# Kernel optimization log

Measured on AMD Instinct MI355X. Metric: run time of the kernel, lower is better.

## Reference

```python
import jax, jax.numpy as jnp
import numpy as np

MARGIN = 0.1
N_SUBSETS = 3
NEG_INF = -1e30


def setup_inputs() -> dict:
    key = jax.random.key(0)
    k1, k2 = jax.random.split(key)
    B, D = 12288, 128
    emb = jax.random.normal(k1, (B, D), dtype=jnp.float32)
    emb = emb / jnp.linalg.norm(emb, axis=-1, keepdims=True)  # cosine-style sims in [-1,1]
    target = jax.random.randint(k2, (B,), 0, 512, dtype=jnp.int64)
    return {"emb": emb, "target": target}


def _subset_loss(e, t):
    # e: [m, D], t: [m]
    m = e.shape[0]
    sim = e @ e.T                                   # [m, m]
    same = t[:, None] == t[None, :]
    eye = jnp.eye(m, dtype=bool)
    pos = same & ~eye                                # positives, diagonal excluded
    neg = ~same                                      # negatives (diag is 'same', so excluded)
    max_neg = jnp.max(jnp.where(neg, sim, NEG_INF), axis=1)   # neg_pair_[-1]
    max_pos = jnp.max(jnp.where(pos, sim, NEG_INF), axis=1)   # pos_pair_[-1]
    # select pos sims < max_neg + margin; loss = sum(1 - pos)
    pos_sel = pos & (sim < (max_neg + MARGIN)[:, None])
    pos_loss = jnp.sum(jnp.where(pos_sel, 1.0 - sim, 0.0), axis=1)
    # select neg sims > max(0.6, max_pos) - margin; loss = sum(neg)
    thr = jnp.maximum(jnp.float32(0.6), max_pos) - MARGIN
    neg_sel = neg & (sim > thr[:, None])
    neg_loss = jnp.sum(jnp.where(neg_sel, sim, 0.0), axis=1)
    has_pos = jnp.any(pos, axis=1)
    row_loss = jnp.where(has_pos, pos_loss + neg_loss, 0.0)
    return jnp.mean(row_loss)  # sum(loss)/n


def reference(emb, target):
    B, D = emb.shape
    m = B // N_SUBSETS
    e = emb.reshape(N_SUBSETS, m, D)
    t = target.reshape(N_SUBSETS, m)
    losses = jax.vmap(_subset_loss)(e, t)  # [n_subsets]
    return jnp.mean(losses)
```

## Files before the change

### kernel.cpp

```cpp
#include <hip/hip_runtime.h>
#include <stdint.h>

typedef __bf16 bf16x8 __attribute__((ext_vector_type(8)));
typedef float f32x4 __attribute__((ext_vector_type(4)));
typedef unsigned short ushort8v __attribute__((ext_vector_type(8)));

static constexpr int SUBSETS = 3;
static constexpr int M = 4096;
static constexpr int D = 128;

static constexpr int WG_ROWS = 256;
static constexpr int WG_COLS = 256;
static constexpr int NSTRIP = M / WG_COLS;
static constexpr int NPANEL = M / WG_ROWS;
static constexpr int WGS = SUBSETS * NPANEL * NSTRIP;
static constexpr int SCOLS = 32;
static constexpr int NSTAGE = WG_COLS / SCOLS;

#define MARGIN_F 0.1f
#define NEGINF (-1e30f)
#define POSINF (1e30f)

__global__ void cvt_f32_bf16(const float* __restrict__ in,
                             unsigned short* __restrict__ out, int n8,
                             float* __restrict__ loss_out) {
    int i = blockIdx.x * blockDim.x + threadIdx.x;
    if (i == 0) *loss_out = 0.0f;
    if (i >= n8) return;
    const float4* p = reinterpret_cast<const float4*>(in) + (size_t)i * 2;
    float4 a = p[0];
    float4 b = p[1];
    float v[8] = {a.x, a.y, a.z, a.w, b.x, b.y, b.z, b.w};
    ushort8v r;
#pragma unroll
    for (int j = 0; j < 8; ++j) {
        uint32_t u = __builtin_bit_cast(uint32_t, v[j]);
        u = (u + 0x7FFFu + ((u >> 16) & 1u)) >> 16;
        r[j] = (unsigned short)u;
    }
    *(reinterpret_cast<ushort8v*>(out) + i) = r;
}

__device__ __forceinline__ void stage_tile(const unsigned short* __restrict__ base,
                                           unsigned short* __restrict__ ldsbuf,
                                           int w, int lane) {
#pragma unroll
    for (int i = 0; i < 2; ++i) {
        const int slocal = w * 2048 + i * 1024 + lane * 16;
        const int col = slocal >> 8;
        const int off = (slocal & 255) ^ ((col & 7) << 4);
        const char* gsrc = (const char*)base + col * 256 + off;
        char* ldst = (char*)ldsbuf + w * 2048 + i * 1024;
        __builtin_amdgcn_global_load_lds(
            (const __attribute__((address_space(1))) void*)gsrc,
            (__attribute__((address_space(3))) void*)ldst,
            16, 0, 0);
    }
}

__device__ __forceinline__ bf16x8 lds_bfrag(const unsigned short* __restrict__ ldsbuf,
                                            int tt, int llo, int lhi, int kb) {
    const int col = tt * 16 + llo;
    const int off = (kb * 64 + lhi * 16) ^ ((col & 7) << 4);
    return *reinterpret_cast<const bf16x8*>((const char*)ldsbuf + col * 256 + off);
}

__global__ __launch_bounds__(256) void pass_max(
        const unsigned short* __restrict__ ebf,
        const int* __restrict__ tgt,
        float* __restrict__ wsmax) {
    __shared__ unsigned short lds[2][SCOLS * D];

    const int wg = blockIdx.x;
    const int s = wg >> 8;
    const int rem = wg & 255;
    const int panel = rem & (NPANEL - 1);
    const int cs = rem >> 4;

    const int tid = threadIdx.x;
    const int w = tid >> 6, lane = tid & 63;
    const int lhi = lane >> 4, llo = lane & 15;

    const unsigned short* E = ebf + (size_t)s * M * D;
    const int* T = tgt + s * M;
    const int rowBase = panel * WG_ROWS + w * 64;
    const int colBase = cs * WG_COLS;

    stage_tile(E + (size_t)colBase * D, lds[0], w, lane);

    bf16x8 a[4][4];
#pragma unroll
    for (int rr = 0; rr < 4; ++rr) {
        const int row = rowBase + rr * 16 + llo;
#pragma unroll
        for (int kb = 0; kb < 4; ++kb)
            a[rr][kb] = *reinterpret_cast<const bf16x8*>(
                E + (size_t)row * D + kb * 32 + lhi * 8);
    }
    int trow[4][4];
#pragma unroll
    for (int rr = 0; rr < 4; ++rr)
#pragma unroll
        for (int r = 0; r < 4; ++r)
            trow[rr][r] = T[rowBase + rr * 16 + lhi * 4 + r];

    float mp[4][4], mn[4][4];
#pragma unroll
    for (int rr = 0; rr < 4; ++rr)
#pragma unroll
        for (int r = 0; r < 4; ++r) { mp[rr][r] = NEGINF; mn[rr][r] = NEGINF; }

    __syncthreads();

    for (int st = 0; st < NSTAGE; ++st) {
        const int buf = st & 1;
        if (st + 1 < NSTAGE)
            stage_tile(E + (size_t)(colBase + (st + 1) * SCOLS) * D, lds[buf ^ 1], w, lane);
#pragma unroll
        for (int tt = 0; tt < 2; ++tt) {
            const int bcol = colBase + st * SCOLS + tt * 16 + llo;
            bf16x8 b[4];
#pragma unroll
            for (int kb = 0; kb < 4; ++kb) b[kb] = lds_bfrag(lds[buf], tt, llo, lhi, kb);
            const int tcol = T[bcol];
#pragma unroll
            for (int rr = 0; rr < 4; ++rr) {
                f32x4 acc = {0.f, 0.f, 0.f, 0.f};
#pragma unroll
                for (int kb = 0; kb < 4; ++kb)
                    acc = __builtin_amdgcn_mfma_f32_16x16x32_bf16(a[rr][kb], b[kb], acc, 0, 0, 0);
#pragma unroll
                for (int r = 0; r < 4; ++r) {
                    const float sv = acc[r];
                    const int rowG = rowBase + rr * 16 + lhi * 4 + r;
                    const bool same = (tcol == trow[rr][r]);
                    const bool offd = (rowG != bcol);
                    mp[rr][r] = fmaxf(mp[rr][r], (same && offd) ? sv : NEGINF);
                    mn[rr][r] = fmaxf(mn[rr][r], same ? NEGINF : sv);
                }
            }
        }
        __syncthreads();
    }

#pragma unroll
    for (int rr = 0; rr < 4; ++rr)
#pragma unroll
        for (int r = 0; r < 4; ++r) {
#pragma unroll
            for (int off = 1; off < 16; off <<= 1) {
                mp[rr][r] = fmaxf(mp[rr][r], __shfl_xor(mp[rr][r], off));
                mn[rr][r] = fmaxf(mn[rr][r], __shfl_xor(mn[rr][r], off));
            }
        }
    if (llo == 0) {
#pragma unroll
        for (int rr = 0; rr < 4; ++rr)
#pragma unroll
            for (int r = 0; r < 4; ++r) {
                const int row = rowBase + rr * 16 + lhi * 4 + r;
                wsmax[((size_t)(0 * SUBSETS + s) * M + row) * NSTRIP + cs] = mp[rr][r];
                wsmax[((size_t)(1 * SUBSETS + s) * M + row) * NSTRIP + cs] = mn[rr][r];
            }
    }
}

__global__ __launch_bounds__(256) void pass_sum(
        const unsigned short* __restrict__ ebf,
        const int* __restrict__ tgt,
        const float* __restrict__ wsmax,
        float* __restrict__ out) {
    __shared__ unsigned short lds[2][SCOLS * D];
    __shared__ float wsum[4];

    const int wg = blockIdx.x;
    const int s = wg >> 8;
    const int rem = wg & 255;
    const int panel = rem & (NPANEL - 1);
    const int cs = rem >> 4;

    const int tid = threadIdx.x;
    const int w = tid >> 6, lane = tid & 63;
    const int lhi = lane >> 4, llo = lane & 15;

    const unsigned short* E = ebf + (size_t)s * M * D;
    const int* T = tgt + s * M;
    const int rowBase = panel * WG_ROWS + w * 64;
    const int colBase = cs * WG_COLS;

    stage_tile(E + (size_t)colBase * D, lds[0], w, lane);

    float thrP[4][4], thrN[4][4];
#pragma unroll
    for (int rr = 0; rr < 4; ++rr)
#pragma unroll
        for (int r = 0; r < 4; ++r) {
            const int row = rowBase + rr * 16 + lhi * 4 + r;
            float vp = wsmax[((size_t)(0 * SUBSETS + s) * M + row) * NSTRIP + llo];
            float vn = wsmax[((size_t)(1 * SUBSETS + s) * M + row) * NSTRIP + llo];
#pragma unroll
            for (int off = 1; off < 16; off <<= 1) {
                vp = fmaxf(vp, __shfl_xor(vp, off));
                vn = fmaxf(vn, __shfl_xor(vn, off));
            }
            const bool hasPos = (vp > -1e29f);
            thrP[rr][r] = hasPos ? vn + MARGIN_F : NEGINF;
            thrN[rr][r] = hasPos ? fmaxf(0.6f, vp) - MARGIN_F : POSINF;
        }

    bf16x8 a[4][4];
#pragma unroll
    for (int rr = 0; rr < 4; ++rr) {
        const int row = rowBase + rr * 16 + llo;
#pragma unroll
        for (int kb = 0; kb < 4; ++kb)
            a[rr][kb] = *reinterpret_cast<const bf16x8*>(
                E + (size_t)row * D + kb * 32 + lhi * 8);
    }
    int trow[4][4];
#pragma unroll
    for (int rr = 0; rr < 4; ++rr)
#pragma unroll
        for (int r = 0; r < 4; ++r)
            trow[rr][r] = T[rowBase + rr * 16 + lhi * 4 + r];

    float acl[4][4];
#pragma unroll
    for (int rr = 0; rr < 4; ++rr)
#pragma unroll
        for (int r = 0; r < 4; ++r) acl[rr][r] = 0.f;

    __syncthreads();

    for (int st = 0; st < NSTAGE; ++st) {
        const int buf = st & 1;
        if (st + 1 < NSTAGE)
            stage_tile(E + (size_t)(colBase + (st + 1) * SCOLS) * D, lds[buf ^ 1], w, lane);
#pragma unroll
        for (int tt = 0; tt < 2; ++tt) {
            const int bcol = colBase + st * SCOLS + tt * 16 + llo;
            bf16x8 b[4];
#pragma unroll
            for (int kb = 0; kb < 4; ++kb) b[kb] = lds_bfrag(lds[buf], tt, llo, lhi, kb);
            const int tcol = T[bcol];
#pragma unroll
            for (int rr = 0; rr < 4; ++rr) {
                f32x4 acc = {0.f, 0.f, 0.f, 0.f};
#pragma unroll
                for (int kb = 0; kb < 4; ++kb)
                    acc = __builtin_amdgcn_mfma_f32_16x16x32_bf16(a[rr][kb], b[kb], acc, 0, 0, 0);
#pragma unroll
                for (int r = 0; r < 4; ++r) {
                    const float sv = acc[r];
                    const int rowG = rowBase + rr * 16 + lhi * 4 + r;
                    const bool same = (tcol == trow[rr][r]);
                    const bool offd = (rowG != bcol);
                    const float addp = (same && offd && (sv < thrP[rr][r])) ? (1.0f - sv) : 0.0f;
                    const float addn = (!same && (sv > thrN[rr][r])) ? sv : 0.0f;
                    acl[rr][r] += addp + addn;
                }
            }
        }
        __syncthreads();
    }

    float tot = 0.f;
#pragma unroll
    for (int rr = 0; rr < 4; ++rr)
#pragma unroll
        for (int r = 0; r < 4; ++r) tot += acl[rr][r];
#pragma unroll
    for (int off = 1; off < 64; off <<= 1) tot += __shfl_xor(tot, off);

    if (lane == 0) wsum[w] = tot;
    __syncthreads();
    if (tid == 0)
        atomicAdd(out, (wsum[0] + wsum[1] + wsum[2] + wsum[3]) * (1.0f / 12288.0f));
}

extern "C" void kernel_launch(void* const* d_in, const int* in_sizes, int n_in,
                              void* d_out, int out_size, void* d_ws, size_t ws_size,
                              hipStream_t stream) {
    const float* emb = (const float*)d_in[0];
    const int* tgt = (const int*)d_in[1];
    float* out = (float*)d_out;

    unsigned short* ebf = (unsigned short*)d_ws;
    float* wsmax = (float*)((char*)d_ws + (size_t)SUBSETS * M * D * 2);

    const int n = SUBSETS * M * D;
    const int n8 = n / 8;

    cvt_f32_bf16<<<n8 / 256, 256, 0, stream>>>(emb, ebf, n8, out);
    pass_max<<<WGS, 256, 0, stream>>>(ebf, tgt, wsmax);
    pass_sum<<<WGS, 256, 0, stream>>>(ebf, tgt, wsmax, out);
}
```

Before: 126.2 us.

## Drop LDS staging; load B fragments directly from global with register double-buffering

Removes the shared-memory tile staging and workgroup barriers in both passes; each wave now independently loads its column fragments straight from global memory (relying on L1/L2 caching) with a two-deep register prefetch, and waves in a workgroup no longer share a column strip. Occupancy hint of 3 blocks per SIMD is added and the per-block LDS reduction is replaced with a per-wave atomicAdd. It aims to remove barrier stalls and LDS traffic, at the cost of redundant global/L2 reads of the B tiles, more atomics, and less data reuse across waves.

```diff
diff --git a/kernel.cpp b/kernel.cpp
--- a/kernel.cpp
+++ b/kernel.cpp
@@ -9,13 +9,13 @@
 static constexpr int M = 4096;
 static constexpr int D = 128;
 
-static constexpr int WG_ROWS = 256;
-static constexpr int WG_COLS = 256;
-static constexpr int NSTRIP = M / WG_COLS;
-static constexpr int NPANEL = M / WG_ROWS;
-static constexpr int WGS = SUBSETS * NPANEL * NSTRIP;
-static constexpr int SCOLS = 32;
-static constexpr int NSTAGE = WG_COLS / SCOLS;
+static constexpr int RPW = 64;
+static constexpr int CPW = 256;
+static constexpr int NSTRIP = M / CPW;
+static constexpr int NRJ = M / RPW;
+static constexpr int WAVES_TOTAL = SUBSETS * NRJ * NSTRIP;
+static constexpr int WGS = WAVES_TOTAL / 4;
+static constexpr int NST = CPW / 16;
 
 #define MARGIN_F 0.1f
 #define NEGINF (-1e30f)
@@ -41,52 +41,22 @@
     *(reinterpret_cast<ushort8v*>(out) + i) = r;
 }
 
-__device__ __forceinline__ void stage_tile(const unsigned short* __restrict__ base,
-                                           unsigned short* __restrict__ ldsbuf,
-                                           int w, int lane) {
-#pragma unroll
-    for (int i = 0; i < 2; ++i) {
-        const int slocal = w * 2048 + i * 1024 + lane * 16;
-        const int col = slocal >> 8;
-        const int off = (slocal & 255) ^ ((col & 7) << 4);
-        const char* gsrc = (const char*)base + col * 256 + off;
-        char* ldst = (char*)ldsbuf + w * 2048 + i * 1024;
-        __builtin_amdgcn_global_load_lds(
-            (const __attribute__((address_space(1))) void*)gsrc,
-            (__attribute__((address_space(3))) void*)ldst,
-            16, 0, 0);
-    }
-}
-
-__device__ __forceinline__ bf16x8 lds_bfrag(const unsigned short* __restrict__ ldsbuf,
-                                            int tt, int llo, int lhi, int kb) {
-    const int col = tt * 16 + llo;
-    const int off = (kb * 64 + lhi * 16) ^ ((col & 7) << 4);
-    return *reinterpret_cast<const bf16x8*>((const char*)ldsbuf + col * 256 + off);
-}
-
-__global__ __launch_bounds__(256) void pass_max(
+__global__ __launch_bounds__(256, 3) void pass_max(
         const unsigned short* __restrict__ ebf,
         const int* __restrict__ tgt,
         float* __restrict__ wsmax) {
-    __shared__ unsigned short lds[2][SCOLS * D];
-
-    const int wg = blockIdx.x;
-    const int s = wg >> 8;
-    const int rem = wg & 255;
-    const int panel = rem & (NPANEL - 1);
-    const int cs = rem >> 4;
-
-    const int tid = threadIdx.x;
-    const int w = tid >> 6, lane = tid & 63;
+    const int gwid = blockIdx.x * 4 + (threadIdx.x >> 6);
+    const int lane = threadIdx.x & 63;
+    const int s = gwid >> 10;
+    const int rem = gwid & 1023;
+    const int rj = rem & (NRJ - 1);
+    const int cs = rem >> 6;
     const int lhi = lane >> 4, llo = lane & 15;
 
     const unsigned short* E = ebf + (size_t)s * M * D;
     const int* T = tgt + s * M;
-    const int rowBase = panel * WG_ROWS + w * 64;
-    const int colBase = cs * WG_COLS;
-
-    stage_tile(E + (size_t)colBase * D, lds[0], w, lane);
+    const int rowBase = rj * RPW;
+    const int colBase = cs * CPW;
 
     bf16x8 a[4][4];
 #pragma unroll
@@ -110,37 +80,44 @@
 #pragma unroll
         for (int r = 0; r < 4; ++r) { mp[rr][r] = NEGINF; mn[rr][r] = NEGINF; }
 
-    __syncthreads();
-
-    for (int st = 0; st < NSTAGE; ++st) {
-        const int buf = st & 1;
-        if (st + 1 < NSTAGE)
-            stage_tile(E + (size_t)(colBase + (st + 1) * SCOLS) * D, lds[buf ^ 1], w, lane);
-#pragma unroll
-        for (int tt = 0; tt < 2; ++tt) {
-            const int bcol = colBase + st * SCOLS + tt * 16 + llo;
-            bf16x8 b[4];
-#pragma unroll
-            for (int kb = 0; kb < 4; ++kb) b[kb] = lds_bfrag(lds[buf], tt, llo, lhi, kb);
-            const int tcol = T[bcol];
-#pragma unroll
-            for (int rr = 0; rr < 4; ++rr) {
-                f32x4 acc = {0.f, 0.f, 0.f, 0.f};
-#pragma unroll
-                for (int kb = 0; kb < 4; ++kb)
-                    acc = __builtin_amdgcn_mfma_f32_16x16x32_bf16(a[rr][kb], b[kb], acc, 0, 0, 0);
-#pragma unroll
-                for (int r = 0; r < 4; ++r) {
-                    const float sv = acc[r];
-                    const int rowG = rowBase + rr * 16 + lhi * 4 + r;
-                    const bool same = (tcol == trow[rr][r]);
-                    const bool offd = (rowG != bcol);
-                    mp[rr][r] = fmaxf(mp[rr][r], (same && offd) ? sv : NEGINF);
-                    mn[rr][r] = fmaxf(mn[rr][r], same ? NEGINF : sv);
-                }
-            }
-        }
-        __syncthreads();
+    auto loadB = [&](bf16x8 (&dst)[4], int st) {
+        const unsigned short* bp = E + (size_t)(colBase + st * 16 + llo) * D + lhi * 8;
+#pragma unroll
+        for (int kb = 0; kb < 4; ++kb)
+            dst[kb] = *reinterpret_cast<const bf16x8*>(bp + kb * 32);
+    };
+    auto proc = [&](int st, bf16x8 (&b)[4], int tcol) {
+        const int bcol = colBase + st * 16 + llo;
+#pragma unroll
+        for (int rr = 0; rr < 4; ++rr) {
+            f32x4 acc = {0.f, 0.f, 0.f, 0.f};
+#pragma unroll
+            for (int kb = 0; kb < 4; ++kb)
+                acc = __builtin_amdgcn_mfma_f32_16x16x32_bf16(a[rr][kb], b[kb], acc, 0, 0, 0);
+#pragma unroll
+            for (int r = 0; r < 4; ++r) {
+                const float sv = acc[r];
+                const int rowG = rowBase + rr * 16 + lhi * 4 + r;
+                const bool same = (tcol == trow[rr][r]);
+                const bool offd = (rowG != bcol);
+                mp[rr][r] = fmaxf(mp[rr][r], (same && offd) ? sv : NEGINF);
+                mn[rr][r] = fmaxf(mn[rr][r], same ? NEGINF : sv);
+            }
+        }
+    };
+
+    bf16x8 bA[4], bB[4];
+    int tcA, tcB;
+    loadB(bA, 0);
+    tcA = T[colBase + llo];
+#pragma unroll
+    for (int st2 = 0; st2 < NST; st2 += 2) {
+        if (st2 + 1 < NST) { loadB(bB, st2 + 1); tcB = T[colBase + (st2 + 1) * 16 + llo]; }
+        proc(st2, bA, tcA);
+        if (st2 + 1 < NST) {
+            if (st2 + 2 < NST) { loadB(bA, st2 + 2); tcA = T[colBase + (st2 + 2) * 16 + llo]; }
+            proc(st2 + 1, bB, tcB);
+        }
     }
 
 #pragma unroll
@@ -165,30 +142,23 @@
     }
 }
 
-__global__ __launch_bounds__(256) void pass_sum(
+__global__ __launch_bounds__(256, 3) void pass_sum(
         const unsigned short* __restrict__ ebf,
         const int* __restrict__ tgt,
         const float* __restrict__ wsmax,
         float* __restrict__ out) {
-    __shared__ unsigned short lds[2][SCOLS * D];
-    __shared__ float wsum[4];
-
-    const int wg = blockIdx.x;
-    const int s = wg >> 8;
-    const int rem = wg & 255;
-    const int panel = rem & (NPANEL - 1);
-    const int cs = rem >> 4;
-
-    const int tid = threadIdx.x;
-    const int w = tid >> 6, lane = tid & 63;
+    const int gwid = blockIdx.x * 4 + (threadIdx.x >> 6);
+    const int lane = threadIdx.x & 63;
+    const int s = gwid >> 10;
+    const int rem = gwid & 1023;
+    const int rj = rem & (NRJ - 1);
+    const int cs = rem >> 6;
     const int lhi = lane >> 4, llo = lane & 15;
 
     const unsigned short* E = ebf + (size_t)s * M * D;
     const int* T = tgt + s * M;
-    const int rowBase = panel * WG_ROWS + w * 64;
-    const int colBase = cs * WG_COLS;
-
-    stage_tile(E + (size_t)colBase * D, lds[0], w, lane);
+    const int rowBase = rj * RPW;
+    const int colBase = cs * CPW;
 
     float thrP[4][4], thrN[4][4];
 #pragma unroll
@@ -224,58 +194,52 @@
         for (int r = 0; r < 4; ++r)
             trow[rr][r] = T[rowBase + rr * 16 + lhi * 4 + r];
 
-    float acl[4][4];
-#pragma unroll
-    for (int rr = 0; rr < 4; ++rr)
-#pragma unroll
-        for (int r = 0; r < 4; ++r) acl[rr][r] = 0.f;
-
-    __syncthreads();
-
-    for (int st = 0; st < NSTAGE; ++st) {
-        const int buf = st & 1;
-        if (st + 1 < NSTAGE)
-            stage_tile(E + (size_t)(colBase + (st + 1) * SCOLS) * D, lds[buf ^ 1], w, lane);
-#pragma unroll
-        for (int tt = 0; tt < 2; ++tt) {
-            const int bcol = colBase + st * SCOLS + tt * 16 + llo;
-            bf16x8 b[4];
-#pragma unroll
-            for (int kb = 0; kb < 4; ++kb) b[kb] = lds_bfrag(lds[buf], tt, llo, lhi, kb);
-            const int tcol = T[bcol];
-#pragma unroll
-            for (int rr = 0; rr < 4; ++rr) {
-                f32x4 acc = {0.f, 0.f, 0.f, 0.f};
-#pragma unroll
-                for (int kb = 0; kb < 4; ++kb)
-                    acc = __builtin_amdgcn_mfma_f32_16x16x32_bf16(a[rr][kb], b[kb], acc, 0, 0, 0);
-#pragma unroll
-                for (int r = 0; r < 4; ++r) {
-                    const float sv = acc[r];
-                    const int rowG = rowBase + rr * 16 + lhi * 4 + r;
-                    const bool same = (tcol == trow[rr][r]);
-                    const bool offd = (rowG != bcol);
-                    const float addp = (same && offd && (sv < thrP[rr][r])) ? (1.0f - sv) : 0.0f;
-                    const float addn = (!same && (sv > thrN[rr][r])) ? sv : 0.0f;
-                    acl[rr][r] += addp + addn;
-                }
-            }
-        }
-        __syncthreads();
-    }
-
     float tot = 0.f;
-#pragma unroll
-    for (int rr = 0; rr < 4; ++rr)
-#pragma unroll
-        for (int r = 0; r < 4; ++r) tot += acl[rr][r];
+
+    auto loadB = [&](bf16x8 (&dst)[4], int st) {
+        const unsigned short* bp = E + (size_t)(colBase + st * 16 + llo) * D + lhi * 8;
+#pragma unroll
+        for (int kb = 0; kb < 4; ++kb)
+            dst[kb] = *reinterpret_cast<const bf16x8*>(bp + kb * 32);
+    };
+    auto proc = [&](int st, bf16x8 (&b)[4], int tcol) {
+        const int bcol = colBase + st * 16 + llo;
+#pragma unroll
+        for (int rr = 0; rr < 4; ++rr) {
+            f32x4 acc = {0.f, 0.f, 0.f, 0.f};
+#pragma unroll
+            for (int kb = 0; kb < 4; ++kb)
+                acc = __builtin_amdgcn_mfma_f32_16x16x32_bf16(a[rr][kb], b[kb], acc, 0, 0, 0);
+#pragma unroll
+            for (int r = 0; r < 4; ++r) {
+                const float sv = acc[r];
+                const int rowG = rowBase + rr * 16 + lhi * 4 + r;
+                const bool same = (tcol == trow[rr][r]);
+                const bool offd = (rowG != bcol);
+                const float addp = (same && offd && (sv < thrP[rr][r])) ? (1.0f - sv) : 0.0f;
+                const float addn = (!same && (sv > thrN[rr][r])) ? sv : 0.0f;
+                tot += addp + addn;
+            }
+        }
+    };
+
+    bf16x8 bA[4], bB[4];
+    int tcA, tcB;
+    loadB(bA, 0);
+    tcA = T[colBase + llo];
+#pragma unroll
+    for (int st2 = 0; st2 < NST; st2 += 2) {
+        if (st2 + 1 < NST) { loadB(bB, st2 + 1); tcB = T[colBase + (st2 + 1) * 16 + llo]; }
+        proc(st2, bA, tcA);
+        if (st2 + 1 < NST) {
+            if (st2 + 2 < NST) { loadB(bA, st2 + 2); tcA = T[colBase + (st2 + 2) * 16 + llo]; }
+            proc(st2 + 1, bB, tcB);
+        }
+    }
+
 #pragma unroll
     for (int off = 1; off < 64; off <<= 1) tot += __shfl_xor(tot, off);
-
-    if (lane == 0) wsum[w] = tot;
-    __syncthreads();
-    if (tid == 0)
-        atomicAdd(out, (wsum[0] + wsum[1] + wsum[2] + wsum[3]) * (1.0f / 12288.0f));
+    if (lane == 0) atomicAdd(out, tot * (1.0f / 12288.0f));
 }
 
 extern "C" void kernel_launch(void* const* d_in, const int* in_sizes, int n_in,
```

Result: slower. 235.3 us (+86.5%).
